# Kernel tuning notes

Measured on AMD Instinct MI355X. Metric: run time of the kernel, lower is better.

## Reference

```python
import jax, jax.numpy as jnp
import numpy as np

NEG_SLOPE = 0.2
EPS = 1e-16


def setup_inputs() -> dict:
    key = jax.random.key(0)
    k = jax.random.split(key, 6)
    N, K, D_IN, D_OUT = 20000, 32, 256, 256
    nodes = jax.random.normal(k[0], (N, D_IN), dtype=jnp.float32)
    neighbors = jax.random.normal(k[1], (N, K, D_IN), dtype=jnp.float32)
    # xavier-uniform-ish scales for faithfulness to init_params
    lim_w = float(np.sqrt(6.0 / (D_IN + D_OUT)))
    W = jax.random.uniform(k[2], (D_OUT, D_IN), minval=-lim_w, maxval=lim_w, dtype=jnp.float32)
    lim_a = float(np.sqrt(6.0 / (1 + D_OUT)))
    a_src = jax.random.uniform(k[3], (D_OUT,), minval=-lim_a, maxval=lim_a, dtype=jnp.float32)
    a_tgt = jax.random.uniform(k[4], (D_OUT,), minval=-lim_a, maxval=lim_a, dtype=jnp.float32)
    bias = jnp.zeros((D_OUT,), dtype=jnp.float32)
    return {"nodes": nodes, "neighbors": neighbors, "W": W, "a_src": a_src, "a_tgt": a_tgt, "bias": bias}


def reference(nodes, neighbors, W, a_src, a_tgt, bias):
    # GAT layer (num_of_heads=1), eval mode (dropout = identity).
    # nodes: [N, D_in], neighbors: [N, K, D_in]
    nodes_proj = nodes @ W.T                              # [N, D_out]
    scores_t = nodes_proj @ a_tgt                         # [N]
    neigh_proj = jnp.einsum('nkf,of->nko', neighbors, W)  # [N, K, D_out]
    scores_s = neigh_proj @ a_src                         # [N, K]
    e = scores_s + scores_t[:, None]                      # per-edge raw score
    e = jnp.where(e >= 0, e, NEG_SLOPE * e)               # leakyReLU(0.2)
    exp_e = jnp.exp(e)                                    # original uses raw exp (no max-subtract)
    attn = exp_e / (jnp.sum(exp_e, axis=1, keepdims=True) + EPS)  # [N, K]
    out = jnp.einsum('nk,nko->no', attn, neigh_proj)      # weighted sum over neighbors
    out = out + bias
    return jax.nn.elu(out)                                # activation = ELU
```

## Files before the change

### kernel.cpp

```cpp
#include <hip/hip_runtime.h>
#include <math.h>

#define D 256
#define KNB 32
#define RS 264
#define NEG_SLOPE 0.2f

__global__ __launch_bounds__(256) void prep_kernel(
    const float* __restrict__ W, const float* __restrict__ a_src,
    const float* __restrict__ a_tgt, float* __restrict__ ws)
{
    int t = threadIdx.x;
    int b = blockIdx.x;
    float* w_src = ws;
    float* w_tgt = ws + D;
    float* Wt    = ws + 2 * D;
    if (b < D) {
        Wt[b * D + t] = W[t * D + b];
    } else {
        float as = 0.f, at = 0.f;
        for (int o = 0; o < D; ++o) {
            float w = W[o * D + t];
            as = fmaf(a_src[o], w, as);
            at = fmaf(a_tgt[o], w, at);
        }
        w_src[t] = as;
        w_tgt[t] = at;
    }
}

__global__ __launch_bounds__(256) void scores_t_kernel(
    const float* __restrict__ nodes, const float* __restrict__ ws,
    float* __restrict__ scores_t, int N)
{
    const float* w_tgt = ws + D;
    int wid  = threadIdx.x >> 6;
    int lane = threadIdx.x & 63;
    int n = blockIdx.x * 4 + wid;
    if (n >= N) return;
    const float4* row = reinterpret_cast<const float4*>(nodes + (size_t)n * D);
    float4 v = row[lane];
    float4 w = reinterpret_cast<const float4*>(w_tgt)[lane];
    float s = v.x * w.x + v.y * w.y + v.z * w.z + v.w * w.w;
    #pragma unroll
    for (int off = 1; off < 64; off <<= 1) s += __shfl_xor(s, off);
    if (lane == 0) scores_t[n] = s;
}

__global__ __launch_bounds__(256) void attn_agg_kernel(
    const float* __restrict__ neighbors, const float* __restrict__ ws,
    const float* __restrict__ scores_t, float* __restrict__ agg, int N)
{
    __shared__ __align__(16) float sneigh[KNB * RS];
    __shared__ __align__(16) float sw[D];
    __shared__ float sp[KNB];
    __shared__ float sinv;

    int t = threadIdx.x;
    int n = blockIdx.x;

    sw[t] = ws[t];

    const float4* g = reinterpret_cast<const float4*>(neighbors + (size_t)n * (KNB * D));
    #pragma unroll
    for (int i = 0; i < 8; ++i) {
        int v = i * 256 + t;
        int k = v >> 6;
        int c = (v & 63) << 2;
        *reinterpret_cast<float4*>(&sneigh[k * RS + c]) = g[v];
    }
    __syncthreads();

    int k = t >> 3, j = t & 7;
    float s = 0.f;
    #pragma unroll
    for (int i = 0; i < 32; ++i) {
        int f = j + (i << 3);
        s = fmaf(sneigh[k * RS + f], sw[f], s);
    }
    s += __shfl_xor(s, 1);
    s += __shfl_xor(s, 2);
    s += __shfl_xor(s, 4);
    if (j == 0) {
        float e = s + scores_t[n];
        e = (e >= 0.f) ? e : NEG_SLOPE * e;
        sp[k] = __expf(e);
    }
    __syncthreads();

    if (t < 64) {
        float p = (t < KNB) ? sp[t] : 0.f;
        #pragma unroll
        for (int off = 1; off < KNB; off <<= 1) p += __shfl_xor(p, off);
        if (t == 0) sinv = 1.f / (p + 1e-16f);
    }
    __syncthreads();

    float acc = 0.f;
    #pragma unroll
    for (int kk = 0; kk < KNB; ++kk)
        acc = fmaf(sp[kk], sneigh[kk * RS + t], acc);
    agg[(size_t)n * D + t] = acc * sinv;
}

#define TILE 32
__global__ __launch_bounds__(256) void out_kernel(
    float* __restrict__ io, const float* __restrict__ ws,
    const float* __restrict__ bias, int N)
{
    const float* Wt = ws + 2 * D;
    __shared__ __align__(16) float sa[TILE][D];

    int t = threadIdx.x;
    int n0 = blockIdx.x * TILE;

    const float4* g = reinterpret_cast<const float4*>(io + (size_t)n0 * D);
    float4* s4 = reinterpret_cast<float4*>(&sa[0][0]);
    int nvalid4 = (min(TILE, N - n0)) * (D / 4);
    #pragma unroll
    for (int i = 0; i < TILE * D / 1024; ++i) {
        int v = i * 256 + t;
        s4[v] = (v < nvalid4) ? g[v] : make_float4(0.f, 0.f, 0.f, 0.f);
    }
    __syncthreads();

    int to = t & 63;
    int tj = t >> 6;
    const float4* wt4 = reinterpret_cast<const float4*>(Wt);

    float4 acc[8];
    #pragma unroll
    for (int jj = 0; jj < 8; ++jj) acc[jj] = make_float4(0.f, 0.f, 0.f, 0.f);

    for (int f = 0; f < D; ++f) {
        float4 wv = wt4[f * (D / 4) + to];
        #pragma unroll
        for (int jj = 0; jj < 8; ++jj) {
            float a = sa[tj * 8 + jj][f];
            acc[jj].x = fmaf(a, wv.x, acc[jj].x);
            acc[jj].y = fmaf(a, wv.y, acc[jj].y);
            acc[jj].z = fmaf(a, wv.z, acc[jj].z);
            acc[jj].w = fmaf(a, wv.w, acc[jj].w);
        }
    }

    float4 b = reinterpret_cast<const float4*>(bias)[to];
    #pragma unroll
    for (int jj = 0; jj < 8; ++jj) {
        int n = n0 + tj * 8 + jj;
        if (n < N) {
            float4 x;
            x.x = acc[jj].x + b.x;
            x.y = acc[jj].y + b.y;
            x.z = acc[jj].z + b.z;
            x.w = acc[jj].w + b.w;
            x.x = (x.x > 0.f) ? x.x : expm1f(x.x);
            x.y = (x.y > 0.f) ? x.y : expm1f(x.y);
            x.z = (x.z > 0.f) ? x.z : expm1f(x.z);
            x.w = (x.w > 0.f) ? x.w : expm1f(x.w);
            reinterpret_cast<float4*>(io + (size_t)n * D)[to] = x;
        }
    }
}

extern "C" void kernel_launch(void* const* d_in, const int* in_sizes, int n_in,
                              void* d_out, int out_size, void* d_ws, size_t ws_size,
                              hipStream_t stream) {
    const float* nodes     = (const float*)d_in[0];
    const float* neighbors = (const float*)d_in[1];
    const float* W         = (const float*)d_in[2];
    const float* a_src     = (const float*)d_in[3];
    const float* a_tgt     = (const float*)d_in[4];
    const float* bias      = (const float*)d_in[5];
    float* out = (float*)d_out;
    float* ws  = (float*)d_ws;

    int N = in_sizes[0] / D;
    float* scores_t = ws + 2 * D + D * D;

    hipLaunchKernelGGL(prep_kernel, dim3(D + 1), dim3(256), 0, stream,
                       W, a_src, a_tgt, ws);
    hipLaunchKernelGGL(scores_t_kernel, dim3((N + 3) / 4), dim3(256), 0, stream,
                       nodes, ws, scores_t, N);
    hipLaunchKernelGGL(attn_agg_kernel, dim3(N), dim3(256), 0, stream,
                       neighbors, ws, scores_t, out, N);
    hipLaunchKernelGGL(out_kernel, dim3((N + TILE - 1) / TILE), dim3(256), 0, stream,
                       out, ws, bias, N);
}
```

Before: 190.3 us.

## Use bf16 MFMA for output projection and fuse target scores into aggregation

Replaces the fp32 FMA output GEMM with a bf16 MFMA kernel (16x16x32) that reads W and the aggregated features as bf16, removing the transpose of W. It also fuses the target-score dot product into the aggregation kernel and computes source scores while loading neighbors, with wave-level shuffle reductions, which cuts a kernel launch and a barrier stage. The aggregation output is stored as bf16, halving the intermediate traffic. The cost is reduced precision in the projection, and the grid N/16 drops any remainder rows when N is not a multiple of 16.

```diff
diff --git a/kernel.cpp b/kernel.cpp
--- a/kernel.cpp
+++ b/kernel.cpp
@@ -1,10 +1,18 @@
 #include <hip/hip_runtime.h>
+#include <hip/hip_bf16.h>
 #include <math.h>
 
 #define D 256
 #define KNB 32
-#define RS 264
 #define NEG_SLOPE 0.2f
+
+using bfrag = __attribute__((ext_vector_type(8))) short;
+using ffrag = __attribute__((ext_vector_type(4))) float;
+
+__device__ __forceinline__ unsigned short f2bf(float x) {
+    __hip_bfloat16 h = __float2bfloat16(x);
+    return *reinterpret_cast<unsigned short*>(&h);
+}
 
 __global__ __launch_bounds__(256) void prep_kernel(
     const float* __restrict__ W, const float* __restrict__ a_src,
@@ -12,11 +20,12 @@
 {
     int t = threadIdx.x;
     int b = blockIdx.x;
-    float* w_src = ws;
-    float* w_tgt = ws + D;
-    float* Wt    = ws + 2 * D;
-    if (b < D) {
-        Wt[b * D + t] = W[t * D + b];
+    if (b < 64) {
+        const float4* w4 = reinterpret_cast<const float4*>(W);
+        float4 v = w4[b * 256 + t];
+        ushort4 u;
+        u.x = f2bf(v.x); u.y = f2bf(v.y); u.z = f2bf(v.z); u.w = f2bf(v.w);
+        reinterpret_cast<ushort4*>(ws + 512)[b * 256 + t] = u;
     } else {
         float as = 0.f, at = 0.f;
         for (int o = 0; o < D; ++o) {
@@ -24,141 +33,101 @@
             as = fmaf(a_src[o], w, as);
             at = fmaf(a_tgt[o], w, at);
         }
-        w_src[t] = as;
-        w_tgt[t] = at;
+        ws[t]     = as;
+        ws[D + t] = at;
     }
 }
 
-__global__ __launch_bounds__(256) void scores_t_kernel(
-    const float* __restrict__ nodes, const float* __restrict__ ws,
-    float* __restrict__ scores_t, int N)
+__global__ __launch_bounds__(256) void attn_agg_kernel(
+    const float* __restrict__ nodes, const float* __restrict__ neighbors,
+    const float* __restrict__ ws, unsigned short* __restrict__ aggbf, int N)
 {
-    const float* w_tgt = ws + D;
-    int wid  = threadIdx.x >> 6;
-    int lane = threadIdx.x & 63;
-    int n = blockIdx.x * 4 + wid;
-    if (n >= N) return;
-    const float4* row = reinterpret_cast<const float4*>(nodes + (size_t)n * D);
-    float4 v = row[lane];
-    float4 w = reinterpret_cast<const float4*>(w_tgt)[lane];
-    float s = v.x * w.x + v.y * w.y + v.z * w.z + v.w * w.w;
-    #pragma unroll
-    for (int off = 1; off < 64; off <<= 1) s += __shfl_xor(s, off);
-    if (lane == 0) scores_t[n] = s;
-}
-
-__global__ __launch_bounds__(256) void attn_agg_kernel(
-    const float* __restrict__ neighbors, const float* __restrict__ ws,
-    const float* __restrict__ scores_t, float* __restrict__ agg, int N)
-{
-    __shared__ __align__(16) float sneigh[KNB * RS];
-    __shared__ __align__(16) float sw[D];
+    __shared__ __align__(16) float sn[KNB][D];
     __shared__ float sp[KNB];
-    __shared__ float sinv;
 
     int t = threadIdx.x;
     int n = blockIdx.x;
+    int lane = t & 63, w = t >> 6;
 
-    sw[t] = ws[t];
+    float4 wsv = reinterpret_cast<const float4*>(ws)[t & 63];
+
+    float4 nv  = reinterpret_cast<const float4*>(nodes + (size_t)n * D)[lane];
+    float4 wtv = reinterpret_cast<const float4*>(ws + D)[lane];
+    float st = nv.x * wtv.x + nv.y * wtv.y + nv.z * wtv.z + nv.w * wtv.w;
+    #pragma unroll
+    for (int o = 1; o < 64; o <<= 1) st += __shfl_xor(st, o);
 
     const float4* g = reinterpret_cast<const float4*>(neighbors + (size_t)n * (KNB * D));
+    float4* s4 = reinterpret_cast<float4*>(&sn[0][0]);
+    float pk[8];
     #pragma unroll
     for (int i = 0; i < 8; ++i) {
-        int v = i * 256 + t;
-        int k = v >> 6;
-        int c = (v & 63) << 2;
-        *reinterpret_cast<float4*>(&sneigh[k * RS + c]) = g[v];
+        float4 x = g[i * 256 + t];
+        s4[i * 256 + t] = x;
+        pk[i] = x.x * wsv.x + x.y * wsv.y + x.z * wsv.z + x.w * wsv.w;
+    }
+    #pragma unroll
+    for (int i = 0; i < 8; ++i) {
+        #pragma unroll
+        for (int o = 1; o < 64; o <<= 1) pk[i] += __shfl_xor(pk[i], o);
+    }
+    if (lane == 0) {
+        #pragma unroll
+        for (int i = 0; i < 8; ++i) {
+            float e = pk[i] + st;
+            e = (e >= 0.f) ? e : NEG_SLOPE * e;
+            sp[i * 4 + w] = __expf(e);
+        }
     }
     __syncthreads();
 
-    int k = t >> 3, j = t & 7;
-    float s = 0.f;
+    float sum = 0.f, acc = 0.f;
     #pragma unroll
-    for (int i = 0; i < 32; ++i) {
-        int f = j + (i << 3);
-        s = fmaf(sneigh[k * RS + f], sw[f], s);
+    for (int k = 0; k < KNB; ++k) {
+        float p = sp[k];
+        sum += p;
+        acc = fmaf(p, sn[k][t], acc);
     }
-    s += __shfl_xor(s, 1);
-    s += __shfl_xor(s, 2);
-    s += __shfl_xor(s, 4);
-    if (j == 0) {
-        float e = s + scores_t[n];
-        e = (e >= 0.f) ? e : NEG_SLOPE * e;
-        sp[k] = __expf(e);
-    }
-    __syncthreads();
-
-    if (t < 64) {
-        float p = (t < KNB) ? sp[t] : 0.f;
-        #pragma unroll
-        for (int off = 1; off < KNB; off <<= 1) p += __shfl_xor(p, off);
-        if (t == 0) sinv = 1.f / (p + 1e-16f);
-    }
-    __syncthreads();
-
-    float acc = 0.f;
-    #pragma unroll
-    for (int kk = 0; kk < KNB; ++kk)
-        acc = fmaf(sp[kk], sneigh[kk * RS + t], acc);
-    agg[(size_t)n * D + t] = acc * sinv;
+    float r = acc / (sum + 1e-16f);
+    aggbf[(size_t)n * D + t] = f2bf(r);
 }
 
-#define TILE 32
-__global__ __launch_bounds__(256) void out_kernel(
-    float* __restrict__ io, const float* __restrict__ ws,
-    const float* __restrict__ bias, int N)
+__global__ __launch_bounds__(64) void out_gemm_kernel(
+    const unsigned short* __restrict__ aggbf,
+    const unsigned short* __restrict__ wbf,
+    const float* __restrict__ bias, float* __restrict__ out, int N)
 {
-    const float* Wt = ws + 2 * D;
-    __shared__ __align__(16) float sa[TILE][D];
+    int l = threadIdx.x;
+    int m0 = blockIdx.x * 16;
+    if (m0 >= N) return;
+    int lr = l & 15, lk = l >> 4;
 
-    int t = threadIdx.x;
-    int n0 = blockIdx.x * TILE;
+    ffrag acc[16];
+    #pragma unroll
+    for (int nf = 0; nf < 16; ++nf) acc[nf] = ffrag{0.f, 0.f, 0.f, 0.f};
 
-    const float4* g = reinterpret_cast<const float4*>(io + (size_t)n0 * D);
-    float4* s4 = reinterpret_cast<float4*>(&sa[0][0]);
-    int nvalid4 = (min(TILE, N - n0)) * (D / 4);
     #pragma unroll
-    for (int i = 0; i < TILE * D / 1024; ++i) {
-        int v = i * 256 + t;
-        s4[v] = (v < nvalid4) ? g[v] : make_float4(0.f, 0.f, 0.f, 0.f);
-    }
-    __syncthreads();
-
-    int to = t & 63;
-    int tj = t >> 6;
-    const float4* wt4 = reinterpret_cast<const float4*>(Wt);
-
-    float4 acc[8];
-    #pragma unroll
-    for (int jj = 0; jj < 8; ++jj) acc[jj] = make_float4(0.f, 0.f, 0.f, 0.f);
-
-    for (int f = 0; f < D; ++f) {
-        float4 wv = wt4[f * (D / 4) + to];
+    for (int ks = 0; ks < 8; ++ks) {
+        bfrag a = *reinterpret_cast<const bfrag*>(
+            aggbf + (size_t)(m0 + lr) * D + ks * 32 + lk * 8);
         #pragma unroll
-        for (int jj = 0; jj < 8; ++jj) {
-            float a = sa[tj * 8 + jj][f];
-            acc[jj].x = fmaf(a, wv.x, acc[jj].x);
-            acc[jj].y = fmaf(a, wv.y, acc[jj].y);
-            acc[jj].z = fmaf(a, wv.z, acc[jj].z);
-            acc[jj].w = fmaf(a, wv.w, acc[jj].w);
+        for (int nf = 0; nf < 16; ++nf) {
+            bfrag b = *reinterpret_cast<const bfrag*>(
+                wbf + (size_t)(nf * 16 + lr) * D + ks * 32 + lk * 8);
+            acc[nf] = __builtin_amdgcn_mfma_f32_16x16x32_bf16(a, b, acc[nf], 0, 0, 0);
         }
     }
 
-    float4 b = reinterpret_cast<const float4*>(bias)[to];
     #pragma unroll
-    for (int jj = 0; jj < 8; ++jj) {
-        int n = n0 + tj * 8 + jj;
-        if (n < N) {
-            float4 x;
-            x.x = acc[jj].x + b.x;
-            x.y = acc[jj].y + b.y;
-            x.z = acc[jj].z + b.z;
-            x.w = acc[jj].w + b.w;
-            x.x = (x.x > 0.f) ? x.x : expm1f(x.x);
-            x.y = (x.y > 0.f) ? x.y : expm1f(x.y);
-            x.z = (x.z > 0.f) ? x.z : expm1f(x.z);
-            x.w = (x.w > 0.f) ? x.w : expm1f(x.w);
-            reinterpret_cast<float4*>(io + (size_t)n * D)[to] = x;
+    for (int nf = 0; nf < 16; ++nf) {
+        int col = nf * 16 + lr;
+        float bv = bias[col];
+        #pragma unroll
+        for (int r = 0; r < 4; ++r) {
+            int m = m0 + lk * 4 + r;
+            float x = acc[nf][r] + bv;
+            x = (x > 0.f) ? x : expm1f(x);
+            out[(size_t)m * D + col] = x;
         }
     }
 }
@@ -176,14 +145,13 @@
     float* ws  = (float*)d_ws;
 
     int N = in_sizes[0] / D;
-    float* scores_t = ws + 2 * D + D * D;
+    unsigned short* wbf   = (unsigned short*)(ws + 512);
+    unsigned short* aggbf = (unsigned short*)(ws + 33280);
 
-    hipLaunchKernelGGL(prep_kernel, dim3(D + 1), dim3(256), 0, stream,
+    hipLaunchKernelGGL(prep_kernel, dim3(65), dim3(256), 0, stream,
                        W, a_src, a_tgt, ws);
-    hipLaunchKernelGGL(scores_t_kernel, dim3((N + 3) / 4), dim3(256), 0, stream,
-                       nodes, ws, scores_t, N);
     hipLaunchKernelGGL(attn_agg_kernel, dim3(N), dim3(256), 0, stream,
-                       neighbors, ws, scores_t, out, N);
-    hipLaunchKernelGGL(out_kernel, dim3((N + TILE - 1) / TILE), dim3(256), 0, stream,
-                       out, ws, bias, N);
+                       nodes, neighbors, ws, aggbf, N);
+    hipLaunchKernelGGL(out_gemm_kernel, dim3(N / 16), dim3(64), 0, stream,
+                       aggbf, wbf, bias, out, N);
 }
```

After: 184.9 us. 2.9% less time.
